# Optimization experiments

Hardware: AMD Instinct MI355X
Metric: run time of the kernel (lower is better)

Reference implementation:

```python
import jax, jax.numpy as jnp
import numpy as np

GAMMA = 0.1
B, IN_F, FEAT, NCLASS = 4096, 1024, 512, 1000
D = 4 * FEAT  # concatenated feature width


def setup_inputs() -> dict:
    key = jax.random.key(0)
    ks = jax.random.split(key, 9)
    s_in = 1.0 / np.sqrt(IN_F)
    return {
        "x": jax.random.normal(ks[0], (B, IN_F), jnp.float32),
        "x_90": jax.random.normal(ks[1], (B, IN_F), jnp.float32),
        "x_180": jax.random.normal(ks[2], (B, IN_F), jnp.float32),
        "x_270": jax.random.normal(ks[3], (B, IN_F), jnp.float32),
        "W_f": jax.random.uniform(ks[4], (FEAT, IN_F), jnp.float32, -s_in, s_in),
        "b_f": jax.random.uniform(ks[5], (FEAT,), jnp.float32, -s_in, s_in),
        "W_r": jax.random.uniform(ks[6], (FEAT, IN_F), jnp.float32, -s_in, s_in),
        "b_r": jax.random.uniform(ks[7], (FEAT,), jnp.float32, -s_in, s_in),
        "centers": jax.random.normal(ks[8], (NCLASS, D), jnp.float32),
    }


def _forward_feature(x, x90, x180, x270, W_f, b_f, W_r, b_r):
    f = jax.nn.relu(x @ W_f.T + b_f)
    f90 = jax.nn.relu(x90 @ W_r.T + b_r)
    f180 = jax.nn.relu(x180 @ W_r.T + b_r)
    f270 = jax.nn.relu(x270 @ W_r.T + b_r)
    return jnp.concatenate((f, f90, f180, f270), axis=1)  # [B, 4*FEAT]


def _distance_centers(feat, centers):
    # ||f - c||_2 via GEMM trick: ||f||^2 + ||c||^2 - 2 f.c  (same math as
    # the expand/subtract/square/sum/sqrt in the original, w/o B*C*D tensor)
    f2 = jnp.sum(feat * feat, axis=1, keepdims=True)        # [B, 1]
    c2 = jnp.sum(centers * centers, axis=1)                 # [C]
    d2 = f2 + c2[None, :] - 2.0 * (feat @ centers.T)        # [B, C]
    return jnp.sqrt(jnp.maximum(d2, 0.0))


def reference(x, x_90, x_180, x_270, W_f, b_f, W_r, b_r, centers):
    feat = _forward_feature(x, x_90, x_180, x_270, W_f, b_f, W_r, b_r)
    return _distance_centers(feat, centers) * (-GAMMA)  # [B, NCLASS]
```

## Files before the change

kernel.cpp:

```cpp
#include <hip/hip_runtime.h>
#include <hip/hip_bf16.h>

typedef unsigned char u8;
typedef unsigned short u16;
typedef unsigned int u32;
typedef unsigned long long u64;
typedef __attribute__((ext_vector_type(4))) short short4v;
typedef __attribute__((ext_vector_type(4))) int int4v;
typedef __attribute__((ext_vector_type(4))) float f32x4;
typedef __attribute__((ext_vector_type(2))) unsigned int u32x2;

#define BSZ   4096
#define INF   1024
#define FEAT  512
#define NCLS  1000
#define NPAD  1024
#define DTOT  2048
#define SX    32.0f
#define SW    4096.0f
#define SF    32.0f
#define SC    24.0f
#define INV_SXSW 7.62939453125e-6f
#define INV_SFSC (1.0f / 768.0f)

__device__ __forceinline__ u16 f2bf(float f) {
  unsigned int x = __float_as_uint(f);
  x += 0x7fffu + ((x >> 16) & 1u);
  return (u16)(x >> 16);
}
__device__ __forceinline__ float bf2f(u16 h) {
  return __uint_as_float((unsigned int)h << 16);
}
__device__ __forceinline__ u32 pk_i8x4(float a, float b, float c, float d,
                                       float s) {
  int ia = (int)rintf(fminf(fmaxf(a * s, -127.f), 127.f));
  int ib = (int)rintf(fminf(fmaxf(b * s, -127.f), 127.f));
  int ic = (int)rintf(fminf(fmaxf(c * s, -127.f), 127.f));
  int id = (int)rintf(fminf(fmaxf(d * s, -127.f), 127.f));
  return (u32)(ia & 255) | ((u32)(ib & 255) << 8) |
         ((u32)(ic & 255) << 16) | ((u32)(id & 255) << 24);
}
__device__ __forceinline__ void gload_lds16(const void* g, void* l) {
  __builtin_amdgcn_global_load_lds(
      (const __attribute__((address_space(1))) void*)g,
      (__attribute__((address_space(3))) void*)l, 16, 0, 0);
}

__global__ __launch_bounds__(256) void cvt_prep(const float* __restrict__ x0,
                                                const float* __restrict__ x1,
                                                const float* __restrict__ x2,
                                                const float* __restrict__ x3,
                                                const float* __restrict__ W_f,
                                                const float* __restrict__ W_r,
                                                const float* __restrict__ cen,
                                                u8* __restrict__ Xq,
                                                u8* __restrict__ Wq,
                                                u8* __restrict__ Cb,
                                                float* __restrict__ c2) {
  const int b = blockIdx.x;
  const int t = threadIdx.x;
  if (b < 8192) {
    const int q = b >> 11;
    const int i = (b & 2047) * 256 + t;
    const float* in = (q & 2) ? ((q & 1) ? x3 : x2) : ((q & 1) ? x1 : x0);
    const float4* p = (const float4*)in;
    float4 a = p[2 * i], bb = p[2 * i + 1];
    u32x2 o;
    o[0] = pk_i8x4(a.x, a.y, a.z, a.w, SX);
    o[1] = pk_i8x4(bb.x, bb.y, bb.z, bb.w, SX);
    *(u32x2*)&Xq[(size_t)q * BSZ * INF + (size_t)i * 8] = o;
    return;
  }
  if (b < 8704) {
    const int half = (b - 8192) >> 8;
    const int i = ((b - 8192) & 255) * 256 + t;
    const float* in = half ? W_r : W_f;
    const float4* p = (const float4*)in;
    float4 a = p[2 * i], bb = p[2 * i + 1];
    u32x2 o;
    o[0] = pk_i8x4(a.x, a.y, a.z, a.w, SW);
    o[1] = pk_i8x4(bb.x, bb.y, bb.z, bb.w, SW);
    *(u32x2*)&Wq[(size_t)half * FEAT * INF + (size_t)i * 8] = o;
    return;
  }
  const int row = b - 8704;
  float s = 0.f;
  if (row < NCLS) {
    const float4* p = (const float4*)(cen + (size_t)row * DTOT) + 2 * t;
    float4 a = p[0], bb = p[1];
    u32x2 o;
    o[0] = pk_i8x4(a.x, a.y, a.z, a.w, SC);
    o[1] = pk_i8x4(bb.x, bb.y, bb.z, bb.w, SC);
    *(u32x2*)&Cb[(size_t)row * DTOT + t * 8] = o;
#pragma unroll
    for (int q = 0; q < 4; ++q) {
      float f = (float)(int)(signed char)(o[0] >> (8 * q)) * (1.f / SC);
      s += f * f;
    }
#pragma unroll
    for (int q = 0; q < 4; ++q) {
      float f = (float)(int)(signed char)(o[1] >> (8 * q)) * (1.f / SC);
      s += f * f;
    }
  } else {
    u32x2 z = {0, 0};
    *(u32x2*)&Cb[(size_t)row * DTOT + t * 8] = z;
  }
#pragma unroll
  for (int o = 32; o > 0; o >>= 1) s += __shfl_xor(s, o);
  __shared__ float red[4];
  if ((t & 63) == 0) red[t >> 6] = s;
  __syncthreads();
  if (t == 0) c2[row] = red[0] + red[1] + red[2] + red[3];
}

__global__ __launch_bounds__(256) void feat_gemm(const u8* __restrict__ Xq,
                                                 const u8* __restrict__ Wq,
                                                 const float* __restrict__ bf_,
                                                 const float* __restrict__ br_,
                                                 u8* __restrict__ Fb) {
  __shared__ u8 As[2][128 * 128];
  __shared__ u8 Bs[2][128 * 128];
  const int t = threadIdx.x;
  const int lane = t & 63;
  const int wid = t >> 6;
  const int wr = (wid >> 1) * 64;
  const int wc = (wid & 1) * 64;
  const int lid = blockIdx.x;
  const int swg = (lid & 7) * 64 + (lid >> 3);
  const int bm0 = (swg >> 4) * 128;
  const int n  = swg & 15;
  const int gc0 = n * 128;
  const int g = n >> 2;
  const int bn0 = (n & 3) * 128;
  const u8* A = Xq + (size_t)g * BSZ * INF;
  const u8* Bt = Wq + (g ? (size_t)FEAT * INF : 0);
  const float* bias = g ? br_ : bf_;

  const int r32 = t >> 3;
  const int c8 = t & 7;
  const int l15 = lane & 15;
  const int l4 = lane >> 4;

  int4v acc[4][4] = {};

  auto stage = [&](int buf, int k0) {
#pragma unroll
    for (int it = 0; it < 4; ++it) {
      const int row = it * 32 + r32;
      const int sc = (c8 ^ ((row >> 1) & 7)) << 4;
      gload_lds16(&A[(size_t)(bm0 + row) * INF + k0 + sc],
                  &As[buf][row * 128 + c8 * 16]);
      gload_lds16(&Bt[(size_t)(bn0 + row) * INF + k0 + sc],
                  &Bs[buf][row * 128 + c8 * 16]);
    }
  };
  auto comp = [&](int buf) {
#pragma unroll
    for (int kk = 0; kk < 2; ++kk) {
      int4v av[4], bv[4];
#pragma unroll
      for (int i = 0; i < 4; ++i) {
        const int row = wr + i * 16 + l15;
        const int c = (4 * kk + l4) ^ ((row >> 1) & 7);
        av[i] = *(const int4v*)&As[buf][row * 128 + c * 16];
      }
#pragma unroll
      for (int j = 0; j < 4; ++j) {
        const int row = wc + j * 16 + l15;
        const int c = (4 * kk + l4) ^ ((row >> 1) & 7);
        bv[j] = *(const int4v*)&Bs[buf][row * 128 + c * 16];
      }
#pragma unroll
      for (int i = 0; i < 4; ++i)
#pragma unroll
        for (int j = 0; j < 4; ++j)
          acc[i][j] = __builtin_amdgcn_mfma_i32_16x16x64_i8(av[i], bv[j],
                                                            acc[i][j], 0, 0, 0);
    }
  };

  stage(0, 0);
  __syncthreads();
  for (int k0 = 0; k0 < INF; k0 += 256) {
    stage(1, k0 + 128);
    comp(0);
    __syncthreads();
    if (k0 + 256 < INF) stage(0, k0 + 256);
    comp(1);
    __syncthreads();
  }

#pragma unroll
  for (int j = 0; j < 4; ++j) {
    const int col = gc0 + wc + j * 16 + l15;
    const float bval = bias[bn0 + wc + j * 16 + l15];
#pragma unroll
    for (int i = 0; i < 4; ++i) {
      const int rowb = bm0 + wr + i * 16 + l4 * 4;
      float v0 = fmaxf((float)acc[i][j][0] * INV_SXSW + bval, 0.f);
      float v1 = fmaxf((float)acc[i][j][1] * INV_SXSW + bval, 0.f);
      float v2 = fmaxf((float)acc[i][j][2] * INV_SXSW + bval, 0.f);
      float v3 = fmaxf((float)acc[i][j][3] * INV_SXSW + bval, 0.f);
      u32 pk = pk_i8x4(v0, v1, v2, v3, SF);
#pragma unroll
      for (int r = 0; r < 4; ++r)
        Fb[(size_t)(rowb + r) * DTOT + col] = (u8)(pk >> (8 * r));
    }
  }
}

__global__ __launch_bounds__(256) void dist_gemm_sk(const u8* __restrict__ Fb,
                                                    const u8* __restrict__ Cb,
                                                    u16* __restrict__ P) {
  __shared__ u8 As[2][128 * 128];
  __shared__ u8 Bs[2][128 * 128];
  const int t = threadIdx.x;
  const int lane = t & 63;
  const int wid = t >> 6;
  const int wr = (wid >> 1) * 64;
  const int wc = (wid & 1) * 64;
  const int lid = blockIdx.x;
  const int swg = (lid & 7) * 64 + (lid >> 3);
  const int n = swg & 7;
  const int kidx = (swg >> 3) & 1;
  const int bm0 = (swg >> 4) * 128;
  const int bn0 = n * 128;
  const int kbase = kidx * 1024;

  const int r32 = t >> 3;
  const int c8 = t & 7;
  const int l15 = lane & 15;
  const int l4 = lane >> 4;

  int4v acc[4][4] = {};

  auto stage = [&](int buf, int k0) {
#pragma unroll
    for (int it = 0; it < 4; ++it) {
      const int row = it * 32 + r32;
      const int sc = (c8 ^ ((row >> 1) & 7)) << 4;
      gload_lds16(&Fb[(size_t)(bm0 + row) * DTOT + k0 + sc],
                  &As[buf][row * 128 + c8 * 16]);
      gload_lds16(&Cb[(size_t)(bn0 + row) * DTOT + k0 + sc],
                  &Bs[buf][row * 128 + c8 * 16]);
    }
  };
  auto comp = [&](int buf) {
#pragma unroll
    for (int kk = 0; kk < 2; ++kk) {
      int4v av[4], bv[4];
#pragma unroll
      for (int i = 0; i < 4; ++i) {
        const int row = wr + i * 16 + l15;
        const int c = (4 * kk + l4) ^ ((row >> 1) & 7);
        av[i] = *(const int4v*)&As[buf][row * 128 + c * 16];
      }
#pragma unroll
      for (int j = 0; j < 4; ++j) {
        const int row = wc + j * 16 + l15;
        const int c = (4 * kk + l4) ^ ((row >> 1) & 7);
        bv[j] = *(const int4v*)&Bs[buf][row * 128 + c * 16];
      }
#pragma unroll
      for (int i = 0; i < 4; ++i)
#pragma unroll
        for (int j = 0; j < 4; ++j)
          acc[i][j] = __builtin_amdgcn_mfma_i32_16x16x64_i8(av[i], bv[j],
                                                            acc[i][j], 0, 0, 0);
    }
  };

  stage(0, kbase);
  __syncthreads();
  for (int k0 = kbase; k0 < kbase + 1024; k0 += 256) {
    stage(1, k0 + 128);
    comp(0);
    __syncthreads();
    if (k0 + 256 < kbase + 1024) stage(0, k0 + 256);
    comp(1);
    __syncthreads();
  }

  u16* Pk = P + (size_t)kidx * BSZ * NPAD;
#pragma unroll
  for (int j = 0; j < 4; ++j) {
    const int col = bn0 + wc + j * 16 + l15;
#pragma unroll
    for (int i = 0; i < 4; ++i) {
#pragma unroll
      for (int r = 0; r < 4; ++r) {
        const int row = bm0 + wr + i * 16 + l4 * 4 + r;
        Pk[(size_t)row * NPAD + col] = f2bf((float)acc[i][j][r] * INV_SFSC);
      }
    }
  }
}

__global__ __launch_bounds__(256) void combine(const u8* __restrict__ Fb,
                                               const u16* __restrict__ P,
                                               const float* __restrict__ c2,
                                               float* __restrict__ out) {
  const int row = blockIdx.x;
  const int t = threadIdx.x;
  u64 v = *(const u64*)&Fb[(size_t)row * DTOT + t * 8];
  float s = 0.f;
#pragma unroll
  for (int q = 0; q < 8; ++q) {
    float f = (float)((u32)(v >> (8 * q)) & 0xffu) * (1.f / SF);
    s += f * f;
  }
#pragma unroll
  for (int o = 32; o > 0; o >>= 1) s += __shfl_xor(s, o);
  __shared__ float red[4];
  if ((t & 63) == 0) red[t >> 6] = s;
  __syncthreads();
  const float fv = red[0] + red[1] + red[2] + red[3];

  const int c = t * 4;
  if (c >= NCLS) return;
  const short4v p0 = *(const short4v*)&P[(size_t)row * NPAD + c];
  const short4v p1 = *(const short4v*)&P[(size_t)(BSZ + row) * NPAD + c];
  const float4 cv = *(const float4*)&c2[c];
  float4 o;
  o.x = -0.1f * sqrtf(fmaxf(fv + cv.x - 2.f * (bf2f((u16)p0[0]) + bf2f((u16)p1[0])), 0.f));
  o.y = -0.1f * sqrtf(fmaxf(fv + cv.y - 2.f * (bf2f((u16)p0[1]) + bf2f((u16)p1[1])), 0.f));
  o.z = -0.1f * sqrtf(fmaxf(fv + cv.z - 2.f * (bf2f((u16)p0[2]) + bf2f((u16)p1[2])), 0.f));
  o.w = -0.1f * sqrtf(fmaxf(fv + cv.w - 2.f * (bf2f((u16)p0[3]) + bf2f((u16)p1[3])), 0.f));
  *(float4*)&out[(size_t)row * NCLS + c] = o;
}

extern "C" void kernel_launch(void* const* d_in, const int* in_sizes, int n_in,
                              void* d_out, int out_size, void* d_ws, size_t ws_size,
                              hipStream_t stream) {
  const float* x    = (const float*)d_in[0];
  const float* x90  = (const float*)d_in[1];
  const float* x180 = (const float*)d_in[2];
  const float* x270 = (const float*)d_in[3];
  const float* W_f  = (const float*)d_in[4];
  const float* b_f  = (const float*)d_in[5];
  const float* W_r  = (const float*)d_in[6];
  const float* b_r  = (const float*)d_in[7];
  const float* cen  = (const float*)d_in[8];
  float* out = (float*)d_out;

  u8*  Xq = (u8*)d_ws;
  u8*  Wq = Xq + 4ull * BSZ * INF;
  u8*  Cb = Wq + 2ull * FEAT * INF;
  u8*  Fb = Cb + (size_t)NPAD * DTOT;
  u16* P  = (u16*)(Fb + (size_t)BSZ * DTOT);
  float* c2 = (float*)(P + 2ull * BSZ * NPAD);

  cvt_prep<<<9728, 256, 0, stream>>>(x, x90, x180, x270, W_f, W_r, cen,
                                     Xq, Wq, Cb, c2);
  feat_gemm<<<512, 256, 0, stream>>>(Xq, Wq, b_f, b_r, Fb);
  dist_gemm_sk<<<512, 256, 0, stream>>>(Fb, Cb, P);
  combine<<<BSZ, 256, 0, stream>>>(Fb, P, c2, out);
}
```

Before: 55.79 us.

## Fuse distance epilogue into int8 GEMM, drop split-K partials and combine kernel

Replaces the split-K distance GEMM, which wrote bf16 partials to a scratch buffer, and the separate combine kernel with one GEMM over the full K=2048. This GEMM applies the sqrt-distance epilogue directly in registers and writes the fp32 output. Row norms ||f||^2 are computed up front by a small integer pass. The aim is to remove the bf16 partial-sum write and read traffic and one launch. In exchange, each block runs twice as long along K with a narrower 128x64 tile, and output stores are scalar and strided by column.

```diff
diff --git a/kernel.cpp b/kernel.cpp
--- a/kernel.cpp
+++ b/kernel.cpp
@@ -5,9 +5,7 @@
 typedef unsigned short u16;
 typedef unsigned int u32;
 typedef unsigned long long u64;
-typedef __attribute__((ext_vector_type(4))) short short4v;
 typedef __attribute__((ext_vector_type(4))) int int4v;
-typedef __attribute__((ext_vector_type(4))) float f32x4;
 typedef __attribute__((ext_vector_type(2))) unsigned int u32x2;
 
 #define BSZ   4096
@@ -22,15 +20,8 @@
 #define SC    24.0f
 #define INV_SXSW 7.62939453125e-6f
 #define INV_SFSC (1.0f / 768.0f)
-
-__device__ __forceinline__ u16 f2bf(float f) {
-  unsigned int x = __float_as_uint(f);
-  x += 0x7fffu + ((x >> 16) & 1u);
-  return (u16)(x >> 16);
-}
-__device__ __forceinline__ float bf2f(u16 h) {
-  return __uint_as_float((unsigned int)h << 16);
-}
+#define INV_SF2  (1.0f / 1024.0f)
+
 __device__ __forceinline__ u32 pk_i8x4(float a, float b, float c, float d,
                                        float s) {
   int ia = (int)rintf(fminf(fmaxf(a * s, -127.f), 127.f));
@@ -210,30 +201,49 @@
   }
 }
 
-__global__ __launch_bounds__(256) void dist_gemm_sk(const u8* __restrict__ Fb,
-                                                    const u8* __restrict__ Cb,
-                                                    u16* __restrict__ P) {
+__global__ __launch_bounds__(256) void f2_pass(const u8* __restrict__ Fb,
+                                               float* __restrict__ f2) {
+  const int row = blockIdx.x * 4 + (threadIdx.x >> 6);
+  const int lane = threadIdx.x & 63;
+  const u64* p = (const u64*)&Fb[(size_t)row * DTOT];
+  int s = 0;
+#pragma unroll
+  for (int w = 0; w < 4; ++w) {
+    u64 v = p[lane + 64 * w];
+#pragma unroll
+    for (int q = 0; q < 8; ++q) {
+      int bq = (int)((v >> (8 * q)) & 0xffu);
+      s += bq * bq;
+    }
+  }
+#pragma unroll
+  for (int o = 32; o > 0; o >>= 1) s += __shfl_xor(s, o);
+  if (lane == 0) f2[row] = (float)s * INV_SF2;
+}
+
+__global__ __launch_bounds__(256) void dist_fused(const u8* __restrict__ Fb,
+                                                  const u8* __restrict__ Cb,
+                                                  const float* __restrict__ f2,
+                                                  const float* __restrict__ c2,
+                                                  float* __restrict__ out) {
   __shared__ u8 As[2][128 * 128];
-  __shared__ u8 Bs[2][128 * 128];
+  __shared__ u8 Bs[2][64 * 128];
   const int t = threadIdx.x;
   const int lane = t & 63;
   const int wid = t >> 6;
   const int wr = (wid >> 1) * 64;
-  const int wc = (wid & 1) * 64;
+  const int wc = (wid & 1) * 32;
   const int lid = blockIdx.x;
   const int swg = (lid & 7) * 64 + (lid >> 3);
-  const int n = swg & 7;
-  const int kidx = (swg >> 3) & 1;
   const int bm0 = (swg >> 4) * 128;
-  const int bn0 = n * 128;
-  const int kbase = kidx * 1024;
+  const int bn0 = (swg & 15) * 64;
 
   const int r32 = t >> 3;
   const int c8 = t & 7;
   const int l15 = lane & 15;
   const int l4 = lane >> 4;
 
-  int4v acc[4][4] = {};
+  int4v acc[4][2] = {};
 
   auto stage = [&](int buf, int k0) {
 #pragma unroll
@@ -242,6 +252,11 @@
       const int sc = (c8 ^ ((row >> 1) & 7)) << 4;
       gload_lds16(&Fb[(size_t)(bm0 + row) * DTOT + k0 + sc],
                   &As[buf][row * 128 + c8 * 16]);
+    }
+#pragma unroll
+    for (int it = 0; it < 2; ++it) {
+      const int row = it * 32 + r32;
+      const int sc = (c8 ^ ((row >> 1) & 7)) << 4;
       gload_lds16(&Cb[(size_t)(bn0 + row) * DTOT + k0 + sc],
                   &Bs[buf][row * 128 + c8 * 16]);
     }
@@ -249,7 +264,7 @@
   auto comp = [&](int buf) {
 #pragma unroll
     for (int kk = 0; kk < 2; ++kk) {
-      int4v av[4], bv[4];
+      int4v av[4], bv[2];
 #pragma unroll
       for (int i = 0; i < 4; ++i) {
         const int row = wr + i * 16 + l15;
@@ -257,7 +272,7 @@
         av[i] = *(const int4v*)&As[buf][row * 128 + c * 16];
       }
 #pragma unroll
-      for (int j = 0; j < 4; ++j) {
+      for (int j = 0; j < 2; ++j) {
         const int row = wc + j * 16 + l15;
         const int c = (4 * kk + l4) ^ ((row >> 1) & 7);
         bv[j] = *(const int4v*)&Bs[buf][row * 128 + c * 16];
@@ -265,69 +280,41 @@
 #pragma unroll
       for (int i = 0; i < 4; ++i)
 #pragma unroll
-        for (int j = 0; j < 4; ++j)
+        for (int j = 0; j < 2; ++j)
           acc[i][j] = __builtin_amdgcn_mfma_i32_16x16x64_i8(av[i], bv[j],
                                                             acc[i][j], 0, 0, 0);
     }
   };
 
-  stage(0, kbase);
+  stage(0, 0);
   __syncthreads();
-  for (int k0 = kbase; k0 < kbase + 1024; k0 += 256) {
+  for (int k0 = 0; k0 < DTOT; k0 += 256) {
     stage(1, k0 + 128);
     comp(0);
     __syncthreads();
-    if (k0 + 256 < kbase + 1024) stage(0, k0 + 256);
+    if (k0 + 256 < DTOT) stage(0, k0 + 256);
     comp(1);
     __syncthreads();
   }
 
-  u16* Pk = P + (size_t)kidx * BSZ * NPAD;
-#pragma unroll
-  for (int j = 0; j < 4; ++j) {
-    const int col = bn0 + wc + j * 16 + l15;
-#pragma unroll
-    for (int i = 0; i < 4; ++i) {
-#pragma unroll
-      for (int r = 0; r < 4; ++r) {
-        const int row = bm0 + wr + i * 16 + l4 * 4 + r;
-        Pk[(size_t)row * NPAD + col] = f2bf((float)acc[i][j][r] * INV_SFSC);
-      }
-    }
-  }
-}
-
-__global__ __launch_bounds__(256) void combine(const u8* __restrict__ Fb,
-                                               const u16* __restrict__ P,
-                                               const float* __restrict__ c2,
-                                               float* __restrict__ out) {
-  const int row = blockIdx.x;
-  const int t = threadIdx.x;
-  u64 v = *(const u64*)&Fb[(size_t)row * DTOT + t * 8];
-  float s = 0.f;
-#pragma unroll
-  for (int q = 0; q < 8; ++q) {
-    float f = (float)((u32)(v >> (8 * q)) & 0xffu) * (1.f / SF);
-    s += f * f;
-  }
-#pragma unroll
-  for (int o = 32; o > 0; o >>= 1) s += __shfl_xor(s, o);
-  __shared__ float red[4];
-  if ((t & 63) == 0) red[t >> 6] = s;
-  __syncthreads();
-  const float fv = red[0] + red[1] + red[2] + red[3];
-
-  const int c = t * 4;
-  if (c >= NCLS) return;
-  const short4v p0 = *(const short4v*)&P[(size_t)row * NPAD + c];
-  const short4v p1 = *(const short4v*)&P[(size_t)(BSZ + row) * NPAD + c];
-  const float4 cv = *(const float4*)&c2[c];
-  float4 o;
-  o.x = -0.1f * sqrtf(fmaxf(fv + cv.x - 2.f * (bf2f((u16)p0[0]) + bf2f((u16)p1[0])), 0.f));
-  o.y = -0.1f * sqrtf(fmaxf(fv + cv.y - 2.f * (bf2f((u16)p0[1]) + bf2f((u16)p1[1])), 0.f));
-  o.z = -0.1f * sqrtf(fmaxf(fv + cv.z - 2.f * (bf2f((u16)p0[2]) + bf2f((u16)p1[2])), 0.f));
-  o.w = -0.1f * sqrtf(fmaxf(fv + cv.w - 2.f * (bf2f((u16)p0[3]) + bf2f((u16)p1[3])), 0.f));
-  *(float4*)&out[(size_t)row * NCLS + c] = o;
+  const int col0 = bn0 + wc + l15;
+  const int col1 = col0 + 16;
+  const float c2v0 = c2[col0];
+  const float c2v1 = c2[col1];
+#pragma unroll
+  for (int i = 0; i < 4; ++i) {
+#pragma unroll
+    for (int r = 0; r < 4; ++r) {
+      const int row = bm0 + wr + i * 16 + l4 * 4 + r;
+      const float fv = f2[row];
+      float d0 = fv + c2v0 - 2.f * (float)acc[i][0][r] * INV_SFSC;
+      float d1 = fv + c2v1 - 2.f * (float)acc[i][1][r] * INV_SFSC;
+      float v0 = -0.1f * sqrtf(fmaxf(d0, 0.f));
+      float v1 = -0.1f * sqrtf(fmaxf(d1, 0.f));
+      if (col0 < NCLS) out[(size_t)row * NCLS + col0] = v0;
+      if (col1 < NCLS) out[(size_t)row * NCLS + col1] = v1;
+    }
+  }
 }
 
 extern "C" void kernel_launch(void* const* d_in, const int* in_sizes, int n_in,
@@ -348,12 +335,12 @@
   u8*  Wq = Xq + 4ull * BSZ * INF;
   u8*  Cb = Wq + 2ull * FEAT * INF;
   u8*  Fb = Cb + (size_t)NPAD * DTOT;
-  u16* P  = (u16*)(Fb + (size_t)BSZ * DTOT);
-  float* c2 = (float*)(P + 2ull * BSZ * NPAD);
+  float* f2 = (float*)(Fb + (size_t)BSZ * DTOT);
+  float* c2 = f2 + BSZ;
 
   cvt_prep<<<9728, 256, 0, stream>>>(x, x90, x180, x270, W_f, W_r, cen,
                                      Xq, Wq, Cb, c2);
   feat_gemm<<<512, 256, 0, stream>>>(Xq, Wq, b_f, b_r, Fb);
-  dist_gemm_sk<<<512, 256, 0, stream>>>(Fb, Cb, P);
-  combine<<<BSZ, 256, 0, stream>>>(Fb, P, c2, out);
-}
+  f2_pass<<<BSZ / 4, 256, 0, stream>>>(Fb, f2);
+  dist_fused<<<512, 256, 0, stream>>>(Fb, Cb, f2, c2, out);
+}
```

Measured after the change: 59.04 us. 5.8% more time.
